# Performance work log

Measured on AMD Instinct MI355X. Metric: run time of the kernel, lower is better.

Reference implementation:

```python
import jax, jax.numpy as jnp
import numpy as np

N = 4096          # nodes
E = 131072        # edges (avg degree 32)
D_IN = 128        # node_dim
H = 256           # hidden_dim
HEADS = 8
DH = H // HEADS


def setup_inputs() -> dict:
    key = jax.random.key(0)
    ks = jax.random.split(key, 24)
    w = lambda k, shape: (jax.random.normal(k, shape, dtype=jnp.float32) * 0.05)
    inp = {
        "x": jax.random.normal(ks[0], (N, D_IN), dtype=jnp.float32),
        "edge_index": jax.random.randint(ks[1], (2, E), 0, N, dtype=jnp.int32),
        # GCN conv weights (PyG GCNConv: out = aggr(norm * x @ W) + b)
        "W1": w(ks[2], (D_IN, H)), "b1": jnp.zeros((H,), jnp.float32),
        "W2": w(ks[3], (H, H)),    "b2": jnp.zeros((H,), jnp.float32),
        "W3": w(ks[4], (H, H)),    "b3": jnp.zeros((H,), jnp.float32),
        # nn.MultiheadAttention params (torch layout: y = x @ W.T + b)
        "in_w": w(ks[5], (3 * H, H)), "in_b": jnp.zeros((3 * H,), jnp.float32),
        "out_w": w(ks[6], (H, H)),    "out_b": jnp.zeros((H,), jnp.float32),
        # failure_predictor MLP: H -> H/2 -> 3
        "fp1_w": w(ks[7], (H // 2, H)), "fp1_b": jnp.zeros((H // 2,), jnp.float32),
        "fp2_w": w(ks[8], (3, H // 2)), "fp2_b": jnp.zeros((3,), jnp.float32),
        # pattern_detector MLP: H -> H/2 -> 10
        "pd1_w": w(ks[9], (H // 2, H)),  "pd1_b": jnp.zeros((H // 2,), jnp.float32),
        "pd2_w": w(ks[10], (10, H // 2)), "pd2_b": jnp.zeros((10,), jnp.float32),
    }
    return inp


def gcn_conv(x, src, dst, W, b):
    """PyG GCNConv with self-loops and symmetric normalization."""
    h = x @ W                                   # [N, H]
    deg = jnp.zeros((N,), x.dtype).at[dst].add(1.0) + 1.0   # +1 for self-loop
    dinv = jax.lax.rsqrt(deg)
    norm = dinv[src] * dinv[dst]                # [E]
    agg = jnp.zeros_like(h).at[dst].add(h[src] * norm[:, None])
    agg = agg + h * (1.0 / deg)[:, None]        # self-loop term: deg^-1/2 * deg^-1/2
    return agg + b


def mha(h, in_w, in_b, out_w, out_b):
    qkv = h @ in_w.T + in_b                     # [N, 3H]
    q, k, v = jnp.split(qkv, 3, axis=-1)
    q = q.reshape(N, HEADS, DH).transpose(1, 0, 2)   # [h, N, dh]
    k = k.reshape(N, HEADS, DH).transpose(1, 0, 2)
    v = v.reshape(N, HEADS, DH).transpose(1, 0, 2)
    scores = jnp.einsum("hnd,hmd->hnm", q, k) / np.sqrt(DH)
    attn = jax.nn.softmax(scores, axis=-1)
    o = jnp.einsum("hnm,hmd->hnd", attn, v)          # [h, N, dh]
    o = o.transpose(1, 0, 2).reshape(N, H)
    return o @ out_w.T + out_b


def reference(x, edge_index, W1, b1, W2, b2, W3, b3, in_w, in_b, out_w, out_b,
              fp1_w, fp1_b, fp2_w, fp2_b, pd1_w, pd1_b, pd2_w, pd2_b):
    src, dst = edge_index[0], edge_index[1]
    h = jax.nn.relu(gcn_conv(x, src, dst, W1, b1))   # dropout is identity in eval
    h = jax.nn.relu(gcn_conv(h, src, dst, W2, b2))
    h = gcn_conv(h, src, dst, W3, b3)
    h = h + mha(h, in_w, in_b, out_w, out_b)
    risk = jax.nn.softmax(jax.nn.relu(h @ fp1_w.T + fp1_b) @ fp2_w.T + fp2_b, axis=-1)
    patterns = jax.nn.sigmoid(jax.nn.relu(h @ pd1_w.T + pd1_b) @ pd2_w.T + pd2_b)
    return risk, patterns
```

## Files before the change

kernel.cpp:

```cpp
#include <hip/hip_runtime.h>
#include <math.h>

static constexpr int NNODE = 4096;
static constexpr int HDIM  = 256;
static constexpr int DIN   = 128;
static constexpr int HEADS = 8;
static constexpr int SPLIT = 4;

using short8 = __attribute__((ext_vector_type(8))) short;
using f32x4  = __attribute__((ext_vector_type(4))) float;

__device__ inline unsigned short bfr(float x) {
    union { float f; unsigned u; } v; v.f = x;
    unsigned r = v.u + 0x7FFFu + ((v.u >> 16) & 1u);
    return (unsigned short)(r >> 16);
}
__device__ inline float bf2f(unsigned short u) {
    union { unsigned u; float f; } v; v.u = (unsigned)u << 16; return v.f;
}
__device__ inline unsigned cvt_pk_bf16(float lo, float hi) {
    unsigned r;
    asm("v_cvt_pk_bf16_f32 %0, %1, %2" : "=v"(r) : "v"(lo), "v"(hi));
    return r;
}

static constexpr float QSCALE_LOG2 = 0.25503527f;

__global__ void k_deg(const int* __restrict__ ei, int* __restrict__ degi, int E) {
    int e = blockIdx.x * 256 + threadIdx.x;
    if (e < E) atomicAdd(&degi[ei[E + e]], 1);
}

__global__ __launch_bounds__(256) void k_scan_norm(const int* __restrict__ degi,
        int* __restrict__ off, int* __restrict__ cursor,
        float* __restrict__ dinv, float* __restrict__ invdeg) {
    __shared__ int partial[256];
    __shared__ int basesh[256];
    int t = threadIdx.x;
    int local[16];
    int s = 0;
    #pragma unroll
    for (int i = 0; i < 16; ++i) { local[i] = degi[t * 16 + i]; s += local[i]; }
    partial[t] = s;
    __syncthreads();
    if (t == 0) {
        int run = 0;
        for (int i = 0; i < 256; ++i) { basesh[i] = run; run += partial[i]; }
    }
    __syncthreads();
    int b = basesh[t];
    #pragma unroll
    for (int i = 0; i < 16; ++i) {
        int n = t * 16 + i;
        off[n] = b; cursor[n] = b; b += local[i];
        float d = (float)local[i] + 1.0f;
        dinv[n]   = rsqrtf(d);
        invdeg[n] = 1.0f / d;
    }
}

__global__ void k_fill(const int* __restrict__ ei, int* __restrict__ cursor,
                       int* __restrict__ csr, int E) {
    int e = blockIdx.x * 256 + threadIdx.x;
    if (e < E) {
        int d = ei[E + e];
        int p = atomicAdd(&cursor[d], 1);
        csr[p] = ei[e];
    }
}

__global__ __launch_bounds__(256) void k_prep(
        const float* __restrict__ W1, const float* __restrict__ W2,
        const float* __restrict__ W3, const float* __restrict__ in_w,
        const float* __restrict__ outw, const float* __restrict__ fp1w,
        const float* __restrict__ pd1w, const float* __restrict__ fp1b,
        const float* __restrict__ pd1b, const float* __restrict__ x,
        unsigned short* __restrict__ W1t, unsigned short* __restrict__ W2t,
        unsigned short* __restrict__ W3t, unsigned short* __restrict__ in_wb,
        unsigned short* __restrict__ outwb, unsigned short* __restrict__ wcatb,
        float* __restrict__ bcat, unsigned short* __restrict__ xb) {
    int idx = blockIdx.x * 256 + threadIdx.x;
    if (idx < 32768) {
        int c = idx >> 7, k = idx & 127;
        W1t[idx] = bfr(W1[(size_t)k * 256 + c]);
    } else if (idx < 98304) {
        int j = idx - 32768; int c = j >> 8, k = j & 255;
        W2t[j] = bfr(W2[(size_t)k * 256 + c]);
    } else if (idx < 163840) {
        int j = idx - 98304; int c = j >> 8, k = j & 255;
        W3t[j] = bfr(W3[(size_t)k * 256 + c]);
    } else if (idx < 360448) {
        int j = idx - 163840;
        in_wb[j] = bfr(in_w[j]);
    } else if (idx < 425984) {
        int j = idx - 360448;
        outwb[j] = bfr(outw[j]);
    } else if (idx < 491520) {
        int j = idx - 425984;
        int row = j >> 8, k = j & 255;
        wcatb[j] = bfr(row < 128 ? fp1w[(size_t)row * 256 + k]
                                 : pd1w[(size_t)(row - 128) * 256 + k]);
        if (j < 256) bcat[j] = (j < 128) ? fp1b[j] : pd1b[j - 128];
    } else if (idx < 557056) {
        int i = (idx - 491520) * 8;
        float4 a = *(const float4*)&x[i];
        float4 b = *(const float4*)&x[i + 4];
        short8 o;
        o[0]=(short)bfr(a.x); o[1]=(short)bfr(a.y); o[2]=(short)bfr(a.z); o[3]=(short)bfr(a.w);
        o[4]=(short)bfr(b.x); o[5]=(short)bfr(b.y); o[6]=(short)bfr(b.z); o[7]=(short)bfr(b.w);
        *(short8*)&xb[i] = o;
    }
}

template<int K, int EPI, bool BIAS, bool ADD>
__global__ __launch_bounds__(256) void k_bgemm(
        const unsigned short* __restrict__ A, const unsigned short* __restrict__ B,
        const float* __restrict__ bias, const float* __restrict__ addsrc,
        void* __restrict__ P0, void* __restrict__ P1, void* __restrict__ P2,
        int Nout) {
    const int lane = threadIdx.x & 63, wave = threadIdx.x >> 6;
    const int ql = lane & 15, g = lane >> 4;
    const int m0w = blockIdx.y * 64 + wave * 16;
    const int n0 = blockIdx.x * 32;
    const unsigned short* ap = A + (size_t)(m0w + ql) * K + g * 8;
    const unsigned short* bp = B + (size_t)(n0 + ql) * K + g * 8;

    f32x4 acc[2] = {{0,0,0,0},{0,0,0,0}};
    #pragma unroll
    for (int k0 = 0; k0 < K; k0 += 32) {
        short8 a = *(const short8*)(ap + k0);
        #pragma unroll
        for (int nt = 0; nt < 2; ++nt) {
            short8 b = *(const short8*)(bp + (size_t)nt * 16 * K + k0);
            acc[nt] = __builtin_amdgcn_mfma_f32_16x16x32_bf16(a, b, acc[nt], 0, 0, 0);
        }
    }
    #pragma unroll
    for (int nt = 0; nt < 2; ++nt) {
        const int col = n0 + nt * 16 + ql;
        const float bv = BIAS ? bias[col] : 0.f;
        if (EPI == 2) {
            const int sec = col >> 8, cc = col & 255;
            const int head = cc >> 5, dh = cc & 31;
            unsigned short* dst = (unsigned short*)(sec == 0 ? P0 : (sec == 1 ? P1 : P2));
            const float sc = (sec == 0) ? QSCALE_LOG2 : 1.0f;
            #pragma unroll
            for (int i = 0; i < 4; ++i) {
                int row = m0w + g * 4 + i;
                dst[((size_t)head * NNODE + row) * 32 + dh] = bfr((acc[nt][i] + bv) * sc);
            }
        } else if (EPI == 1) {
            unsigned short* Cb = (unsigned short*)P0;
            #pragma unroll
            for (int i = 0; i < 4; ++i) {
                int row = m0w + g * 4 + i;
                float v = acc[nt][i] + bv;
                if (ADD) v += addsrc[(size_t)row * Nout + col];
                Cb[(size_t)row * Nout + col] = bfr(v);
            }
        } else {
            float* Cf = (float*)P0;
            #pragma unroll
            for (int i = 0; i < 4; ++i) {
                int row = m0w + g * 4 + i;
                float v = acc[nt][i] + bv;
                if (ADD) v += addsrc[(size_t)row * Nout + col];
                Cf[(size_t)row * Nout + col] = v;
            }
        }
    }
}

template<int MODE>
__global__ __launch_bounds__(256) void k_gather(const unsigned short* __restrict__ hW,
        const int* __restrict__ csr, const int* __restrict__ off,
        const int* __restrict__ degi, const float* __restrict__ dinv,
        const float* __restrict__ invdeg, const float* __restrict__ bias,
        float* __restrict__ aggf, unsigned short* __restrict__ aggb) {
    const int n = blockIdx.x;
    const int c = threadIdx.x;
    const int start = off[n];
    const int cnt = degi[n];
    __shared__ int   sidx[64];
    __shared__ float swht[64];
    float acc = 0.f;
    for (int k0 = 0; k0 < cnt; k0 += 64) {
        __syncthreads();
        if (c < 64 && k0 + c < cnt) {
            int s = csr[start + k0 + c];
            sidx[c] = s;
            swht[c] = dinv[s];
        }
        __syncthreads();
        int lim = min(64, cnt - k0);
        for (int k = 0; k < lim; ++k)
            acc += bf2f(hW[(size_t)sidx[k] * HDIM + c]) * swht[k];
    }
    float val = acc * dinv[n] + bf2f(hW[(size_t)n * HDIM + c]) * invdeg[n] + bias[c];
    if (MODE == 0) {
        aggb[(size_t)n * HDIM + c] = bfr(fmaxf(val, 0.f));
    } else {
        aggf[(size_t)n * HDIM + c] = val;
        aggb[(size_t)n * HDIM + c] = bfr(val);
    }
}

__global__ __launch_bounds__(256) void k_attn_mfma(const unsigned short* __restrict__ qh,
        const unsigned short* __restrict__ kh, const unsigned short* __restrict__ vh,
        unsigned short* __restrict__ po, float* __restrict__ pm, float* __restrict__ pl) {
    const int hd = blockIdx.x;
    const int qb = blockIdx.y;
    const int z  = blockIdx.z;
    const int tid = threadIdx.x;
    const int wave = tid >> 6, lane = tid & 63;
    const int ql = lane & 15, g = lane >> 4;

    __shared__ unsigned short Vt[2][32 * 72];
    __shared__ unsigned short Plds[4][16 * 72];

    const unsigned short* khh = kh + (size_t)hd * NNODE * 32;
    const unsigned short* vhh = vh + (size_t)hd * NNODE * 32;
    const int row = qb * 64 + wave * 16 + ql;
    short8 qf = *(const short8*)(qh + ((size_t)hd * NNODE + row) * 32 + g * 8);

    f32x4 oa0 = {0,0,0,0}, oa1 = {0,0,0,0};
    float m = -INFINITY, l = 0.f;

    const int vkey = tid & 63, vdh = (tid >> 6) * 8;
    const int TPS = NNODE / 64 / SPLIT;
    const int t0 = z * TPS;

    {
        short8 vv = *(const short8*)(vhh + (size_t)(t0 * 64 + vkey) * 32 + vdh);
        #pragma unroll
        for (int i = 0; i < 8; ++i) Vt[0][(vdh + i) * 72 + vkey] = (unsigned short)vv[i];
    }
    __syncthreads();
    int cur = 0;

    for (int kt = t0; kt < t0 + TPS; ++kt) {
        if (kt + 1 < t0 + TPS) {
            short8 vv = *(const short8*)(vhh + (size_t)((kt + 1) * 64 + vkey) * 32 + vdh);
            #pragma unroll
            for (int i = 0; i < 8; ++i) Vt[cur ^ 1][(vdh + i) * 72 + vkey] = (unsigned short)vv[i];
        }

        f32x4 st[4];
        #pragma unroll
        for (int t = 0; t < 4; ++t) {
            short8 kf = *(const short8*)(khh + (size_t)(kt * 64 + t * 16 + ql) * 32 + g * 8);
            st[t] = __builtin_amdgcn_mfma_f32_16x16x32_bf16(kf, qf, (f32x4){0,0,0,0}, 0, 0, 0);
        }

        float mloc = -INFINITY;
        #pragma unroll
        for (int t = 0; t < 4; ++t)
            mloc = fmaxf(mloc, fmaxf(fmaxf(st[t][0], st[t][1]), fmaxf(st[t][2], st[t][3])));
        mloc = fmaxf(mloc, __shfl_xor(mloc, 16));
        mloc = fmaxf(mloc, __shfl_xor(mloc, 32));

        if (!__all(mloc <= m + 8.f)) {
            float mnew = fmaxf(m, mloc);
            float corr = exp2f(m - mnew);
            l *= corr; oa0 *= corr; oa1 *= corr; m = mnew;
        }

        float ll = 0.f;
        unsigned pw[8];
        #pragma unroll
        for (int t = 0; t < 4; ++t) {
            float p0 = exp2f(st[t][0] - m);
            float p1 = exp2f(st[t][1] - m);
            float p2 = exp2f(st[t][2] - m);
            float p3 = exp2f(st[t][3] - m);
            ll += (p0 + p1) + (p2 + p3);
            pw[t * 2 + 0] = cvt_pk_bf16(p0, p1);
            pw[t * 2 + 1] = cvt_pk_bf16(p2, p3);
        }
        ll += __shfl_xor(ll, 16);
        ll += __shfl_xor(ll, 32);
        l += ll;

        #pragma unroll
        for (int t = 0; t < 4; ++t) {
            uint2 w2; w2.x = pw[t * 2 + 0]; w2.y = pw[t * 2 + 1];
            *(uint2*)&Plds[wave][ql * 72 + t * 16 + g * 4] = w2;
        }

        #pragma unroll
        for (int c = 0; c < 2; ++c) {
            short8 pf = *(const short8*)&Plds[wave][ql * 72 + c * 32 + g * 8];
            short8 v0 = *(const short8*)&Vt[cur][ql * 72 + c * 32 + g * 8];
            short8 v1 = *(const short8*)&Vt[cur][(16 + ql) * 72 + c * 32 + g * 8];
            oa0 = __builtin_amdgcn_mfma_f32_16x16x32_bf16(v0, pf, oa0, 0, 0, 0);
            oa1 = __builtin_amdgcn_mfma_f32_16x16x32_bf16(v1, pf, oa1, 0, 0, 0);
        }
        __syncthreads();
        cur ^= 1;
    }

    const size_t pidx = ((size_t)hd * NNODE + row) * SPLIT + z;
    unsigned short* pp = po + pidx * 32;
    uint2 r0, r1;
    r0.x = cvt_pk_bf16(oa0[0], oa0[1]); r0.y = cvt_pk_bf16(oa0[2], oa0[3]);
    r1.x = cvt_pk_bf16(oa1[0], oa1[1]); r1.y = cvt_pk_bf16(oa1[2], oa1[3]);
    *(uint2*)&pp[g * 4]      = r0;
    *(uint2*)&pp[16 + g * 4] = r1;
    if (g == 0) { pm[pidx] = m; pl[pidx] = l; }
}

__global__ __launch_bounds__(256) void k_attn_merge(const unsigned short* __restrict__ po,
        const float* __restrict__ pm, const float* __restrict__ pl,
        unsigned short* __restrict__ ob) {
    int idx = blockIdx.x * 256 + threadIdx.x;
    int row = idx >> 8, c = idx & 255;
    int hd = c >> 5, dh = c & 31;
    size_t b4 = ((size_t)hd * NNODE + row) * SPLIT;
    float m0 = pm[b4+0], m1 = pm[b4+1], m2 = pm[b4+2], m3 = pm[b4+3];
    float M = fmaxf(fmaxf(m0, m1), fmaxf(m2, m3));
    float w0 = exp2f(m0 - M), w1 = exp2f(m1 - M);
    float w2 = exp2f(m2 - M), w3 = exp2f(m3 - M);
    float L = pl[b4]*w0 + pl[b4+1]*w1 + pl[b4+2]*w2 + pl[b4+3]*w3;
    float v = bf2f(po[(b4+0)*32 + dh])*w0 + bf2f(po[(b4+1)*32 + dh])*w1
            + bf2f(po[(b4+2)*32 + dh])*w2 + bf2f(po[(b4+3)*32 + dh])*w3;
    ob[idx] = bfr(v / L);
}

__global__ __launch_bounds__(256) void k_heads2(const float* __restrict__ th,
        const float* __restrict__ fp2w, const float* __restrict__ fp2b,
        const float* __restrict__ pd2w, const float* __restrict__ pd2b,
        float* __restrict__ out) {
    const int wave = threadIdx.x >> 6, lane = threadIdx.x & 63;
    const int n = blockIdx.x * 4 + wave;
    const int half = lane >> 5;
    const int li = lane & 31;
    float4 h4 = *(const float4*)&th[(size_t)n * HDIM + half * 128 + li * 4];
    h4.x = fmaxf(h4.x, 0.f); h4.y = fmaxf(h4.y, 0.f);
    h4.z = fmaxf(h4.z, 0.f); h4.w = fmaxf(h4.w, 0.f);
    float lf[3];
    float lp[10];
    #pragma unroll
    for (int j = 0; j < 10; ++j) {
        float partial = 0.f;
        if (half == 0) {
            if (j < 3) {
                float4 wv = *(const float4*)&fp2w[j * 128 + li * 4];
                partial = h4.x*wv.x + h4.y*wv.y + h4.z*wv.z + h4.w*wv.w;
            }
        } else {
            float4 wv = *(const float4*)&pd2w[j * 128 + li * 4];
            partial = h4.x*wv.x + h4.y*wv.y + h4.z*wv.z + h4.w*wv.w;
        }
        #pragma unroll
        for (int d = 1; d < 32; d <<= 1) partial += __shfl_xor(partial, d);
        if (j < 3) lf[j] = partial;
        lp[j] = partial;
    }
    if (lane == 0) {
        float l0 = lf[0] + fp2b[0], l1 = lf[1] + fp2b[1], l2 = lf[2] + fp2b[2];
        float mx = fmaxf(l0, fmaxf(l1, l2));
        float e0 = __expf(l0 - mx), e1 = __expf(l1 - mx), e2 = __expf(l2 - mx);
        float inv = 1.f / (e0 + e1 + e2);
        out[(size_t)n * 3 + 0] = e0 * inv;
        out[(size_t)n * 3 + 1] = e1 * inv;
        out[(size_t)n * 3 + 2] = e2 * inv;
    } else if (lane == 32) {
        #pragma unroll
        for (int j = 0; j < 10; ++j)
            out[(size_t)NNODE * 3 + (size_t)n * 10 + j] =
                1.f / (1.f + __expf(-(lp[j] + pd2b[j])));
    }
}

extern "C" void kernel_launch(void* const* d_in, const int* in_sizes, int n_in,
                              void* d_out, int out_size, void* d_ws, size_t ws_size,
                              hipStream_t stream) {
    const float* x    = (const float*)d_in[0];
    const int*   ei   = (const int*)  d_in[1];
    const float* W1   = (const float*)d_in[2];
    const float* b1   = (const float*)d_in[3];
    const float* W2   = (const float*)d_in[4];
    const float* b2   = (const float*)d_in[5];
    const float* W3   = (const float*)d_in[6];
    const float* b3   = (const float*)d_in[7];
    const float* in_w = (const float*)d_in[8];
    const float* in_b = (const float*)d_in[9];
    const float* outw = (const float*)d_in[10];
    const float* outb = (const float*)d_in[11];
    const float* fp1w = (const float*)d_in[12];
    const float* fp1b = (const float*)d_in[13];
    const float* fp2w = (const float*)d_in[14];
    const float* fp2b = (const float*)d_in[15];
    const float* pd1w = (const float*)d_in[16];
    const float* pd1b = (const float*)d_in[17];
    const float* pd2w = (const float*)d_in[18];
    const float* pd2b = (const float*)d_in[19];
    float* out = (float*)d_out;

    const int E = in_sizes[1] / 2;

    char* w = (char*)d_ws;
    auto alloc = [&](size_t bytes) {
        char* p = w; w += (bytes + 255) & ~(size_t)255; return p;
    };
    int*   degi   = (int*)alloc(NNODE * 4);
    int*   off    = (int*)alloc(NNODE * 4);
    int*   cursor = (int*)alloc(NNODE * 4);
    int*   csr    = (int*)alloc((size_t)E * 4);
    float* dinv   = (float*)alloc(NNODE * 4);
    float* invdeg = (float*)alloc(NNODE * 4);
    unsigned short* W1t   = (unsigned short*)alloc(256 * 128 * 2);
    unsigned short* W2t   = (unsigned short*)alloc(256 * 256 * 2);
    unsigned short* W3t   = (unsigned short*)alloc(256 * 256 * 2);
    unsigned short* in_wb = (unsigned short*)alloc(768 * 256 * 2);
    unsigned short* outwb = (unsigned short*)alloc(256 * 256 * 2);
    unsigned short* wcatb = (unsigned short*)alloc(256 * 256 * 2);
    float* bcat  = (float*)alloc(256 * 4);
    unsigned short* xb    = (unsigned short*)alloc((size_t)NNODE * DIN * 2);
    float* bufA  = (float*)alloc((size_t)NNODE * HDIM * 4);
    unsigned short* bufAb = (unsigned short*)alloc((size_t)NNODE * HDIM * 2);
    unsigned short* aggb1 = (unsigned short*)alloc((size_t)NNODE * HDIM * 2);
    unsigned short* aggb2 = (unsigned short*)alloc((size_t)NNODE * HDIM * 2);
    float* hf    = (float*)alloc((size_t)NNODE * HDIM * 4);
    unsigned short* hb    = (unsigned short*)alloc((size_t)NNODE * HDIM * 2);
    unsigned short* qh    = (unsigned short*)alloc((size_t)HEADS * NNODE * 32 * 2);
    unsigned short* kh    = (unsigned short*)alloc((size_t)HEADS * NNODE * 32 * 2);
    unsigned short* vh    = (unsigned short*)alloc((size_t)HEADS * NNODE * 32 * 2);
    unsigned short* po    = (unsigned short*)alloc((size_t)HEADS * NNODE * SPLIT * 32 * 2);
    float* pm    = (float*)alloc((size_t)HEADS * NNODE * SPLIT * 4);
    float* pl    = (float*)alloc((size_t)HEADS * NNODE * SPLIT * 4);
    unsigned short* ob    = (unsigned short*)alloc((size_t)NNODE * HDIM * 2);
    unsigned short* hfinb = (unsigned short*)alloc((size_t)NNODE * HDIM * 2);

    hipMemsetAsync(degi, 0, NNODE * sizeof(int), stream);
    k_deg<<<(E + 255) / 256, 256, 0, stream>>>(ei, degi, E);
    k_scan_norm<<<1, 256, 0, stream>>>(degi, off, cursor, dinv, invdeg);
    k_fill<<<(E + 255) / 256, 256, 0, stream>>>(ei, cursor, csr, E);
    k_prep<<<2176, 256, 0, stream>>>(W1, W2, W3, in_w, outw, fp1w, pd1w, fp1b, pd1b, x,
                                     W1t, W2t, W3t, in_wb, outwb, wcatb, bcat, xb);

    dim3 g256(HDIM / 32, NNODE / 64);
    dim3 g768(768 / 32, NNODE / 64);

    k_bgemm<DIN, 1, false, false><<<g256, 256, 0, stream>>>(xb, W1t, nullptr, nullptr, bufAb, nullptr, nullptr, HDIM);
    k_gather<0><<<NNODE, 256, 0, stream>>>(bufAb, csr, off, degi, dinv, invdeg, b1, nullptr, aggb1);
    k_bgemm<HDIM, 1, false, false><<<g256, 256, 0, stream>>>(aggb1, W2t, nullptr, nullptr, bufAb, nullptr, nullptr, HDIM);
    k_gather<0><<<NNODE, 256, 0, stream>>>(bufAb, csr, off, degi, dinv, invdeg, b2, nullptr, aggb2);
    k_bgemm<HDIM, 1, false, false><<<g256, 256, 0, stream>>>(aggb2, W3t, nullptr, nullptr, bufAb, nullptr, nullptr, HDIM);
    k_gather<1><<<NNODE, 256, 0, stream>>>(bufAb, csr, off, degi, dinv, invdeg, b3, hf, hb);

    k_bgemm<HDIM, 2, true, false><<<g768, 256, 0, stream>>>(hb, in_wb, in_b, nullptr, qh, kh, vh, 768);
    k_attn_mfma<<<dim3(HEADS, NNODE / 64, SPLIT), 256, 0, stream>>>(qh, kh, vh, po, pm, pl);
    k_attn_merge<<<(NNODE * HDIM) / 256, 256, 0, stream>>>(po, pm, pl, ob);
    k_bgemm<HDIM, 1, true, true><<<g256, 256, 0, stream>>>(ob, outwb, outb, hf, hfinb, nullptr, nullptr, HDIM);

    k_bgemm<HDIM, 0, true, false><<<g256, 256, 0, stream>>>(hfinb, wcatb, bcat, nullptr, bufA, nullptr, nullptr, HDIM);
    k_heads2<<<NNODE / 4, 256, 0, stream>>>(bufA, fp2w, fp2b, pd2w, pd2b, out);
}
```

Baseline: 206.4 us.

## Write V transposed in QKV epilogue and load it directly in attention

The QKV projection epilogue stores V in a per-head transposed layout (dh-major, nodes contiguous) using packed bf16 stores. The attention kernel then reads V fragments for the PV MFMA directly from global memory instead of double-buffering and transposing tiles through LDS. This removes the LDS transpose writes and the per-tile block barrier, at the cost of unprefetched global/L2 loads on the inner loop.

Result: slower. 245.6 us (+19.0%).

```diff
diff --git a/kernel.cpp b/kernel.cpp
--- a/kernel.cpp
+++ b/kernel.cpp
@@ -142,12 +142,21 @@
         if (EPI == 2) {
             const int sec = col >> 8, cc = col & 255;
             const int head = cc >> 5, dh = cc & 31;
-            unsigned short* dst = (unsigned short*)(sec == 0 ? P0 : (sec == 1 ? P1 : P2));
-            const float sc = (sec == 0) ? QSCALE_LOG2 : 1.0f;
-            #pragma unroll
-            for (int i = 0; i < 4; ++i) {
-                int row = m0w + g * 4 + i;
-                dst[((size_t)head * NNODE + row) * 32 + dh] = bfr((acc[nt][i] + bv) * sc);
+            if (sec == 2) {
+                unsigned short* dst = (unsigned short*)P2
+                    + ((size_t)head * 32 + dh) * NNODE + m0w + g * 4;
+                uint2 pk;
+                pk.x = cvt_pk_bf16(acc[nt][0] + bv, acc[nt][1] + bv);
+                pk.y = cvt_pk_bf16(acc[nt][2] + bv, acc[nt][3] + bv);
+                *(uint2*)dst = pk;
+            } else {
+                unsigned short* dst = (unsigned short*)(sec == 0 ? P0 : P1);
+                const float sc = (sec == 0) ? QSCALE_LOG2 : 1.0f;
+                #pragma unroll
+                for (int i = 0; i < 4; ++i) {
+                    int row = m0w + g * 4 + i;
+                    dst[((size_t)head * NNODE + row) * 32 + dh] = bfr((acc[nt][i] + bv) * sc);
+                }
             }
         } else if (EPI == 1) {
             unsigned short* Cb = (unsigned short*)P0;
@@ -206,7 +215,7 @@
 }
 
 __global__ __launch_bounds__(256) void k_attn_mfma(const unsigned short* __restrict__ qh,
-        const unsigned short* __restrict__ kh, const unsigned short* __restrict__ vh,
+        const unsigned short* __restrict__ kh, const unsigned short* __restrict__ vt,
         unsigned short* __restrict__ po, float* __restrict__ pm, float* __restrict__ pl) {
     const int hd = blockIdx.x;
     const int qb = blockIdx.y;
@@ -215,36 +224,23 @@
     const int wave = tid >> 6, lane = tid & 63;
     const int ql = lane & 15, g = lane >> 4;
 
-    __shared__ unsigned short Vt[2][32 * 72];
     __shared__ unsigned short Plds[4][16 * 72];
 
     const unsigned short* khh = kh + (size_t)hd * NNODE * 32;
-    const unsigned short* vhh = vh + (size_t)hd * NNODE * 32;
+    const unsigned short* vtt = vt + (size_t)hd * 32 * NNODE;
     const int row = qb * 64 + wave * 16 + ql;
     short8 qf = *(const short8*)(qh + ((size_t)hd * NNODE + row) * 32 + g * 8);
 
+    const unsigned short* v0p = vtt + (size_t)ql * NNODE + g * 8;
+    const unsigned short* v1p = vtt + (size_t)(16 + ql) * NNODE + g * 8;
+
     f32x4 oa0 = {0,0,0,0}, oa1 = {0,0,0,0};
     float m = -INFINITY, l = 0.f;
 
-    const int vkey = tid & 63, vdh = (tid >> 6) * 8;
     const int TPS = NNODE / 64 / SPLIT;
     const int t0 = z * TPS;
 
-    {
-        short8 vv = *(const short8*)(vhh + (size_t)(t0 * 64 + vkey) * 32 + vdh);
-        #pragma unroll
-        for (int i = 0; i < 8; ++i) Vt[0][(vdh + i) * 72 + vkey] = (unsigned short)vv[i];
-    }
-    __syncthreads();
-    int cur = 0;
-
     for (int kt = t0; kt < t0 + TPS; ++kt) {
-        if (kt + 1 < t0 + TPS) {
-            short8 vv = *(const short8*)(vhh + (size_t)((kt + 1) * 64 + vkey) * 32 + vdh);
-            #pragma unroll
-            for (int i = 0; i < 8; ++i) Vt[cur ^ 1][(vdh + i) * 72 + vkey] = (unsigned short)vv[i];
-        }
-
         f32x4 st[4];
         #pragma unroll
         for (int t = 0; t < 4; ++t) {
@@ -290,13 +286,11 @@
         #pragma unroll
         for (int c = 0; c < 2; ++c) {
             short8 pf = *(const short8*)&Plds[wave][ql * 72 + c * 32 + g * 8];
-            short8 v0 = *(const short8*)&Vt[cur][ql * 72 + c * 32 + g * 8];
-            short8 v1 = *(const short8*)&Vt[cur][(16 + ql) * 72 + c * 32 + g * 8];
+            short8 v0 = *(const short8*)(v0p + kt * 64 + c * 32);
+            short8 v1 = *(const short8*)(v1p + kt * 64 + c * 32);
             oa0 = __builtin_amdgcn_mfma_f32_16x16x32_bf16(v0, pf, oa0, 0, 0, 0);
             oa1 = __builtin_amdgcn_mfma_f32_16x16x32_bf16(v1, pf, oa1, 0, 0, 0);
         }
-        __syncthreads();
-        cur ^= 1;
     }
 
     const size_t pidx = ((size_t)hd * NNODE + row) * SPLIT + z;
@@ -425,7 +419,7 @@
     unsigned short* hb    = (unsigned short*)alloc((size_t)NNODE * HDIM * 2);
     unsigned short* qh    = (unsigned short*)alloc((size_t)HEADS * NNODE * 32 * 2);
     unsigned short* kh    = (unsigned short*)alloc((size_t)HEADS * NNODE * 32 * 2);
-    unsigned short* vh    = (unsigned short*)alloc((size_t)HEADS * NNODE * 32 * 2);
+    unsigned short* vt    = (unsigned short*)alloc((size_t)HEADS * 32 * NNODE * 2);
     unsigned short* po    = (unsigned short*)alloc((size_t)HEADS * NNODE * SPLIT * 32 * 2);
     float* pm    = (float*)alloc((size_t)HEADS * NNODE * SPLIT * 4);
     float* pl    = (float*)alloc((size_t)HEADS * NNODE * SPLIT * 4);
@@ -449,8 +443,8 @@
     k_bgemm<HDIM, 1, false, false><<<g256, 256, 0, stream>>>(aggb2, W3t, nullptr, nullptr, bufAb, nullptr, nullptr, HDIM);
     k_gather<1><<<NNODE, 256, 0, stream>>>(bufAb, csr, off, degi, dinv, invdeg, b3, hf, hb);
 
-    k_bgemm<HDIM, 2, true, false><<<g768, 256, 0, stream>>>(hb, in_wb, in_b, nullptr, qh, kh, vh, 768);
-    k_attn_mfma<<<dim3(HEADS, NNODE / 64, SPLIT), 256, 0, stream>>>(qh, kh, vh, po, pm, pl);
+    k_bgemm<HDIM, 2, true, false><<<g768, 256, 0, stream>>>(hb, in_wb, in_b, nullptr, qh, kh, vt, 768);
+    k_attn_mfma<<<dim3(HEADS, NNODE / 64, SPLIT), 256, 0, stream>>>(qh, kh, vt, po, pm, pl);
     k_attn_merge<<<(NNODE * HDIM) / 256, 256, 0, stream>>>(po, pm, pl, ob);
     k_bgemm<HDIM, 1, true, true><<<g256, 256, 0, stream>>>(ob, outwb, outb, hf, hfinb, nullptr, nullptr, HDIM);
 
```
